# Optimization experiments

Measured on AMD Instinct MI355X. Metric: run time of the kernel, lower is better.

## Reference

```python
import jax, jax.numpy as jnp
import numpy as np

N = 200_000      # total nodes
E = 3_200_000    # directed edges
F = 128          # input features
G = 2_000        # graphs in batch
SIZES = (128, 128, 128, 128, 128, 64)
K = 2            # TAGConv hops
EPS = 1e-5


def setup_inputs() -> dict:
    key = jax.random.key(0)
    ks = jax.random.split(key, 12)
    x = jax.random.normal(ks[0], (N, F), jnp.float32)
    edge_index = jax.random.randint(ks[1], (2, E), 0, N, dtype=jnp.int32).astype(jnp.int64)
    segment_ids = jnp.sort(jax.random.randint(ks[2], (N,), 0, G, dtype=jnp.int32)).astype(jnp.int64)
    conv_W = jax.random.normal(ks[3], (5, (K + 1) * 128, 128), jnp.float32) * 0.05
    conv_W_last = jax.random.normal(ks[4], ((K + 1) * 128, 64), jnp.float32) * 0.05
    bn_gamma = jnp.ones((5, 128), jnp.float32)
    bn_beta = jnp.zeros((5, 128), jnp.float32)
    bn_gamma_last = jnp.ones((64,), jnp.float32)
    bn_beta_last = jnp.zeros((64,), jnp.float32)
    agg_bn_gamma = jnp.ones((4,), jnp.float32)
    agg_bn_beta = jnp.zeros((4,), jnp.float32)
    agg_W = jax.random.normal(ks[5], (64, 4 * 64), jnp.float32) * 0.05
    agg_b = jnp.zeros((64,), jnp.float32)
    out_W = jax.random.normal(ks[6], (1, 64), jnp.float32) * 0.05
    out_b = jnp.zeros((1,), jnp.float32)
    return dict(x=x, edge_index=edge_index, segment_ids=segment_ids, conv_W=conv_W,
                conv_W_last=conv_W_last, bn_gamma=bn_gamma, bn_beta=bn_beta,
                bn_gamma_last=bn_gamma_last, bn_beta_last=bn_beta_last,
                agg_bn_gamma=agg_bn_gamma, agg_bn_beta=agg_bn_beta,
                agg_W=agg_W, agg_b=agg_b, out_W=out_W, out_b=out_b)


def _forward(x, edge_index, segment_ids, conv_W, conv_W_last, bn_gamma, bn_beta,
             bn_gamma_last, bn_beta_last, agg_bn_gamma, agg_bn_beta,
             agg_W, agg_b, out_W, out_b):
    src, dst = edge_index[0], edge_index[1]
    deg = jax.ops.segment_sum(jnp.ones((E,), x.dtype), dst, num_segments=N)
    norm = jnp.where(deg > 0, jax.lax.rsqrt(jnp.maximum(deg, 1.0)), 0.0)[:, None]  # D^{-1/2}

    def prop(h):  # h: [N, d] -> D^{-1/2} A D^{-1/2} h
        return norm * jax.ops.segment_sum((h * norm)[src], dst, num_segments=N)

    def tagconv(h, W):  # concat of A_norm^k h for k=0..K, then linear (no bias; BN follows)
        hs = [h]
        for _ in range(K):
            hs.append(prop(hs[-1]))
        return jnp.concatenate(hs, axis=-1) @ W

    def bn(h, g, b):  # training-mode batchnorm over nodes
        m = h.mean(0)
        v = h.var(0)
        return (h - m) * jax.lax.rsqrt(v + EPS) * g + b

    outs = []
    h = x
    for l in range(len(SIZES)):
        if l < 5:
            W, g, b = conv_W[l], bn_gamma[l], bn_beta[l]
        else:
            W, g, b = conv_W_last, bn_gamma_last, bn_beta_last
        h = jax.nn.relu(bn(tagconv(h, W), g, b))
        if l >= 2 and SIZES[l] == SIZES[l - 2]:  # skip connection
            h = h + outs[l - 2]
        outs.append(h)

    # ragged pooling: (max, min, mean, std) per graph
    counts = jax.ops.segment_sum(jnp.ones((N,), h.dtype), segment_ids, num_segments=G)[:, None]
    s = jax.ops.segment_sum(h, segment_ids, num_segments=G)
    mean = s / jnp.maximum(counts, 1.0)
    ssq = jax.ops.segment_sum(h * h, segment_ids, num_segments=G)
    var = (ssq - counts * mean * mean) / jnp.maximum(counts - 1.0, 1.0)  # unbiased like th.std
    std = jnp.sqrt(jnp.maximum(var, 0.0))
    mx = jax.ops.segment_max(h, segment_ids, num_segments=G)
    mn = jax.ops.segment_min(h, segment_ids, num_segments=G)
    pooled = jnp.stack([mx, mn, mean, std], axis=1)  # [G, 4, 64]

    # aggregation BatchNorm1d over the 4 pooling channels (stats over graphs x feat)
    m = pooled.mean(axis=(0, 2))
    v = pooled.var(axis=(0, 2))
    pooled = (pooled - m[None, :, None]) * jax.lax.rsqrt(v + EPS)[None, :, None] \
             * agg_bn_gamma[None, :, None] + agg_bn_beta[None, :, None]

    flat = pooled.reshape(G, 4 * SIZES[-1])
    hg = flat @ agg_W.T + agg_b           # aggregation Linear(256 -> 64)
    return hg @ out_W.T + out_b           # output Linear(64 -> 1), shape [G, 1]


def reference(x, edge_index, segment_ids, conv_W, conv_W_last, bn_gamma, bn_beta,
              bn_gamma_last, bn_beta_last, agg_bn_gamma, agg_bn_beta,
              agg_W, agg_b, out_W, out_b):
    return _forward(x, edge_index, segment_ids, conv_W, conv_W_last, bn_gamma, bn_beta,
                    bn_gamma_last, bn_beta_last, agg_bn_gamma, agg_bn_beta,
                    agg_W, agg_b, out_W, out_b)
```

## Files before the change

### kernel.cpp

```cpp
#include <hip/hip_runtime.h>
#include <cstddef>
#include <cstdint>

#define N_NODES  200000
#define N_EDGES  3200000
#define N_GRAPHS 2000
#define BN_EPS   1e-5f
#define NB       391
#define BSH      9
#define CHUNK    16384

typedef unsigned int   u32;
typedef unsigned short u16;

using short8   = __attribute__((ext_vector_type(8))) short;
using floatx16 = __attribute__((ext_vector_type(16))) float;

__device__ __forceinline__ float bflo(u32 v) { union {u32 i; float f;} c; c.i = v << 16; return c.f; }
__device__ __forceinline__ float bfhi(u32 v) { union {u32 i; float f;} c; c.i = v & 0xffff0000u; return c.f; }
__device__ __forceinline__ float bf1(u16 v)  { union {u32 i; float f;} c; c.i = ((u32)v) << 16; return c.f; }
__device__ __forceinline__ u32 f2bf(float f) {
    union {float f; u32 i;} c; c.f = f;
    return (c.i + 0x7fffu + ((c.i >> 16) & 1u)) >> 16;
}
__device__ __forceinline__ u32 pack2(float a, float b) { return f2bf(a) | (f2bf(b) << 16); }

__global__ void x2bf_kernel(const float* __restrict__ x, u16* __restrict__ xb, int total4) {
    for (int i = blockIdx.x * 256 + threadIdx.x; i < total4; i += gridDim.x * 256) {
        float4 v = ((const float4*)x)[i];
        uint2 o; o.x = pack2(v.x, v.y); o.y = pack2(v.z, v.w);
        ((uint2*)xb)[i] = o;
    }
}

__global__ void wpack_all(const float* __restrict__ convW, const float* __restrict__ convWlast,
                          u16* __restrict__ whi, u16* __restrict__ wlo) {
    const int PER = 384 * 128;
    int tid = blockIdx.x * 256 + threadIdx.x;
    float w;
    int dst;
    if (tid < 5 * PER) {
        int l = tid / PER, r = tid % PER;
        int k = r / 128, nn = r % 128;
        w = convW[tid];
        dst = l * PER + (k >> 6) * 128 * 64 + nn * 64 + (k & 63);
    } else {
        int r = tid - 5 * PER;
        if (r >= 384 * 64) return;
        int k = r / 64, nn = r % 64;
        w = convWlast[r];
        dst = 5 * PER + (k >> 6) * 64 * 64 + nn * 64 + (k & 63);
    }
    u16 hi = (u16)f2bf(w);
    float rem = w - bf1(hi);
    whi[dst] = hi;
    wlo[dst] = (u16)f2bf(rem);
}

__global__ __launch_bounds__(256)
void bucket_hist(const int* __restrict__ edst, int* __restrict__ bcnt, int e) {
    __shared__ int h[NB];
    for (int t = threadIdx.x; t < NB; t += 256) h[t] = 0;
    __syncthreads();
    int base = blockIdx.x * CHUNK;
    int end  = min(base + CHUNK, e);
    for (int i = base + threadIdx.x; i < end; i += 256)
        atomicAdd(&h[edst[i] >> BSH], 1);
    __syncthreads();
    for (int t = threadIdx.x; t < NB; t += 256)
        if (h[t]) atomicAdd(&bcnt[t], h[t]);
}

__global__ void bucket_scan(const int* __restrict__ bcnt, int* __restrict__ bbase,
                            int* __restrict__ bcur) {
    __shared__ int ls[512];
    int t = threadIdx.x;
    int v = (t < NB) ? bcnt[t] : 0;
    ls[t] = v;
    __syncthreads();
    for (int off = 1; off < 512; off <<= 1) {
        int a = (t >= off) ? ls[t - off] : 0;
        __syncthreads();
        ls[t] += a;
        __syncthreads();
    }
    if (t <= NB) {
        int excl = ls[t] - v;
        bbase[t] = excl;
        if (t < NB) bcur[t] = excl;
    }
}

__global__ __launch_bounds__(256)
void bucket_scatter(const int* __restrict__ esrc, const int* __restrict__ edst,
                    int* __restrict__ bcur, uint2* __restrict__ esorted, int e) {
    __shared__ int h[NB], lbase[NB], lcur[NB];
    for (int t = threadIdx.x; t < NB; t += 256) { h[t] = 0; lcur[t] = 0; }
    __syncthreads();
    int base = blockIdx.x * CHUNK;
    int end  = min(base + CHUNK, e);
    for (int i = base + threadIdx.x; i < end; i += 256)
        atomicAdd(&h[edst[i] >> BSH], 1);
    __syncthreads();
    for (int t = threadIdx.x; t < NB; t += 256)
        lbase[t] = h[t] ? atomicAdd(&bcur[t], h[t]) : 0;
    __syncthreads();
    for (int i = base + threadIdx.x; i < end; i += 256) {
        int d = edst[i];
        int b = d >> BSH;
        int p = lbase[b] + atomicAdd(&lcur[b], 1);
        uint2 ed; ed.x = (u32)esrc[i]; ed.y = (u32)d;
        esorted[p] = ed;
    }
}

__global__ __launch_bounds__(256)
void bucket_fill(const uint2* __restrict__ esorted, const int* __restrict__ bbase,
                 int* __restrict__ rowptr, int* __restrict__ csr,
                 float* __restrict__ normv, int n, int e) {
    __shared__ int cnt[512], loc[512], tsum[256];
    const int b = blockIdx.x;
    const int ebeg = bbase[b], eend = bbase[b + 1];
    const int t = threadIdx.x;
    cnt[t] = 0; cnt[t + 256] = 0;
    __syncthreads();
    for (int i = ebeg + t; i < eend; i += 256)
        atomicAdd(&cnt[esorted[i].y & 511], 1);
    __syncthreads();
    int c0 = cnt[2 * t], c1 = cnt[2 * t + 1];
    tsum[t] = c0 + c1;
    __syncthreads();
    for (int off = 1; off < 256; off <<= 1) {
        int a = (t >= off) ? tsum[t - off] : 0;
        __syncthreads();
        tsum[t] += a;
        __syncthreads();
    }
    int excl = tsum[t] - (c0 + c1);
    loc[2 * t] = excl;
    loc[2 * t + 1] = excl + c0;
    __syncthreads();
    for (int j = t; j < 512; j += 256) {
        int node = (b << 9) + j;
        if (node < n) {
            rowptr[node] = ebeg + loc[j];
            int deg = cnt[j];
            normv[node] = (deg > 0) ? rsqrtf((float)deg) : 0.f;
        }
    }
    if (b == 0 && t == 0) rowptr[n] = e;
    __syncthreads();
    for (int j = t; j < 512; j += 256) cnt[j] = loc[j];
    __syncthreads();
    for (int i = ebeg + t; i < eend; i += 256) {
        uint2 ed = esorted[i];
        int slot = ebeg + atomicAdd(&cnt[ed.y & 511], 1);
        csr[slot] = (int)ed.x;
    }
}

__global__ __launch_bounds__(256)
void prop_kernel(const u16* __restrict__ hin, const float* __restrict__ norm,
                 const int* __restrict__ rowptr, const int* __restrict__ csr,
                 u16* __restrict__ pout, int n) {
    int wave = threadIdx.x >> 6;
    int lane = threadIdx.x & 63;
    int node = blockIdx.x * 4 + wave;
    if (node >= n) return;
    const int q = lane >> 4;
    const int f = (lane & 15) * 8;
    int s = rowptr[node], e = rowptr[node + 1];
    float a0 = 0, a1 = 0, a2 = 0, a3 = 0, a4 = 0, a5 = 0, a6 = 0, a7 = 0;
    int i = s + q;
    if (i + 12 < e) {
        int sn0 = csr[i], sn1 = csr[i + 4], sn2 = csr[i + 8], sn3 = csr[i + 12];
        while (true) {
            float nw0 = norm[sn0], nw1 = norm[sn1], nw2 = norm[sn2], nw3 = norm[sn3];
            uint4 v0 = *(const uint4*)(hin + (size_t)sn0 * 128 + f);
            uint4 v1 = *(const uint4*)(hin + (size_t)sn1 * 128 + f);
            uint4 v2 = *(const uint4*)(hin + (size_t)sn2 * 128 + f);
            uint4 v3 = *(const uint4*)(hin + (size_t)sn3 * 128 + f);
            int ni = i + 16;
            bool more = (ni + 12 < e);
            int t0 = 0, t1 = 0, t2 = 0, t3 = 0;
            if (more) {
                t0 = csr[ni]; t1 = csr[ni + 4]; t2 = csr[ni + 8]; t3 = csr[ni + 12];
            }
            a0 += bflo(v0.x) * nw0 + bflo(v1.x) * nw1 + bflo(v2.x) * nw2 + bflo(v3.x) * nw3;
            a1 += bfhi(v0.x) * nw0 + bfhi(v1.x) * nw1 + bfhi(v2.x) * nw2 + bfhi(v3.x) * nw3;
            a2 += bflo(v0.y) * nw0 + bflo(v1.y) * nw1 + bflo(v2.y) * nw2 + bflo(v3.y) * nw3;
            a3 += bfhi(v0.y) * nw0 + bfhi(v1.y) * nw1 + bfhi(v2.y) * nw2 + bfhi(v3.y) * nw3;
            a4 += bflo(v0.z) * nw0 + bflo(v1.z) * nw1 + bflo(v2.z) * nw2 + bflo(v3.z) * nw3;
            a5 += bfhi(v0.z) * nw0 + bfhi(v1.z) * nw1 + bfhi(v2.z) * nw2 + bfhi(v3.z) * nw3;
            a6 += bflo(v0.w) * nw0 + bflo(v1.w) * nw1 + bflo(v2.w) * nw2 + bflo(v3.w) * nw3;
            a7 += bfhi(v0.w) * nw0 + bfhi(v1.w) * nw1 + bfhi(v2.w) * nw2 + bfhi(v3.w) * nw3;
            i = ni;
            if (!more) break;
            sn0 = t0; sn1 = t1; sn2 = t2; sn3 = t3;
        }
    }
    for (; i < e; i += 4) {
        int sn0 = csr[i];
        float nw0 = norm[sn0];
        uint4 v0 = *(const uint4*)(hin + (size_t)sn0 * 128 + f);
        a0 += bflo(v0.x) * nw0; a1 += bfhi(v0.x) * nw0;
        a2 += bflo(v0.y) * nw0; a3 += bfhi(v0.y) * nw0;
        a4 += bflo(v0.z) * nw0; a5 += bfhi(v0.z) * nw0;
        a6 += bflo(v0.w) * nw0; a7 += bfhi(v0.w) * nw0;
    }
    a0 += __shfl_down(a0, 32, 64); a1 += __shfl_down(a1, 32, 64);
    a2 += __shfl_down(a2, 32, 64); a3 += __shfl_down(a3, 32, 64);
    a4 += __shfl_down(a4, 32, 64); a5 += __shfl_down(a5, 32, 64);
    a6 += __shfl_down(a6, 32, 64); a7 += __shfl_down(a7, 32, 64);
    a0 += __shfl_down(a0, 16, 64); a1 += __shfl_down(a1, 16, 64);
    a2 += __shfl_down(a2, 16, 64); a3 += __shfl_down(a3, 16, 64);
    a4 += __shfl_down(a4, 16, 64); a5 += __shfl_down(a5, 16, 64);
    a6 += __shfl_down(a6, 16, 64); a7 += __shfl_down(a7, 16, 64);
    if (q == 0) {
        float nd = norm[node];
        uint4 o;
        o.x = pack2(a0 * nd, a1 * nd);
        o.y = pack2(a2 * nd, a3 * nd);
        o.z = pack2(a4 * nd, a5 * nd);
        o.w = pack2(a6 * nd, a7 * nd);
        *(uint4*)(pout + (size_t)node * 128 + f) = o;
    }
}

template <int DOUT>
__global__ __launch_bounds__(256)
void gemm_mfma(const u16* __restrict__ A0, const u16* __restrict__ A1,
               const u16* __restrict__ A2, const u16* __restrict__ whi,
               const u16* __restrict__ wlo, u16* __restrict__ outp,
               float* __restrict__ gstats, int n) {
    constexpr int TJ = DOUT / 64;
    constexpr int BELEMS = DOUT * 64;
    __shared__ u16 As[128 * 64];
    __shared__ u16 Bh[BELEMS];
    __shared__ u16 Bl[BELEMS];
    __shared__ float col_s[DOUT];
    __shared__ float col_q[DOUT];

    const int tid  = threadIdx.x;
    const int wave = tid >> 6;
    const int lane = tid & 63;
    const int wrow = wave >> 1;
    const int wcol = wave & 1;
    const int row0 = blockIdx.x * 128;
    const int m    = lane & 31;
    const int half = lane >> 5;

    const u16* mats[3] = {A0, A1, A2};

    floatx16 acc[2][TJ];
#pragma unroll
    for (int ti = 0; ti < 2; ++ti)
#pragma unroll
        for (int tj = 0; tj < TJ; ++tj)
#pragma unroll
            for (int r = 0; r < 16; ++r) acc[ti][tj][r] = 0.f;

    for (int c = 0; c < 6; ++c) {
        const u16* M = mats[c >> 1];
        const int kloc = (c & 1) * 64;
#pragma unroll
        for (int it = 0; it < 4; ++it) {
            int rib  = wave * 32 + it * 8 + (lane >> 3);
            int grow = row0 + rib;
            if (grow >= n) grow = n - 1;
            uint4 v = *(const uint4*)(M + (size_t)grow * 128 + kloc + (lane & 7) * 8);
            int cc = (lane & 7) ^ (rib & 7);
            *(uint4*)&As[rib * 64 + cc * 8] = v;
        }
        {
            const int cbase = c * BELEMS;
#pragma unroll
            for (int j = 0; j < BELEMS / 2048; ++j) {
                int idx  = tid + j * 256;
                int nrow = idx >> 3, seg = idx & 7;
                int dcc  = seg ^ (nrow & 7);
                *(uint4*)&Bh[nrow * 64 + dcc * 8] =
                    *(const uint4*)(whi + cbase + idx * 8);
                *(uint4*)&Bl[nrow * 64 + dcc * 8] =
                    *(const uint4*)(wlo + cbase + idx * 8);
            }
        }
        __syncthreads();
#pragma unroll
        for (int s = 0; s < 4; ++s) {
            const int cc = s * 2 + half;
            short8 a[2], bhf[TJ], blf[TJ];
#pragma unroll
            for (int ti = 0; ti < 2; ++ti) {
                int r = wrow * 64 + ti * 32 + m;
                a[ti] = *(const short8*)&As[r * 64 + ((cc ^ (r & 7)) * 8)];
            }
#pragma unroll
            for (int tj = 0; tj < TJ; ++tj) {
                int rr = wcol * TJ * 32 + tj * 32 + m;
                int off = rr * 64 + ((cc ^ (rr & 7)) * 8);
                bhf[tj] = *(const short8*)&Bh[off];
                blf[tj] = *(const short8*)&Bl[off];
            }
#pragma unroll
            for (int ti = 0; ti < 2; ++ti)
#pragma unroll
                for (int tj = 0; tj < TJ; ++tj) {
                    acc[ti][tj] = __builtin_amdgcn_mfma_f32_32x32x16_bf16(
                        a[ti], bhf[tj], acc[ti][tj], 0, 0, 0);
                    acc[ti][tj] = __builtin_amdgcn_mfma_f32_32x32x16_bf16(
                        a[ti], blf[tj], acc[ti][tj], 0, 0, 0);
                }
        }
        __syncthreads();
    }

    if (tid < DOUT) { col_s[tid] = 0.f; col_q[tid] = 0.f; }
    __syncthreads();
#pragma unroll
    for (int tj = 0; tj < TJ; ++tj) {
        int gcol = (wcol * TJ + tj) * 32 + m;
        float s = 0.f, qq = 0.f;
#pragma unroll
        for (int ti = 0; ti < 2; ++ti)
#pragma unroll
            for (int r = 0; r < 16; ++r) {
                int grow = row0 + wrow * 64 + ti * 32 + (r & 3) + 8 * (r >> 2) + 4 * half;
                if (grow < n) {
                    float v = acc[ti][tj][r];
                    s += v; qq += v * v;
                    outp[(size_t)grow * DOUT + gcol] = (u16)f2bf(v);
                }
            }
        atomicAdd(&col_s[gcol], s);
        atomicAdd(&col_q[gcol], qq);
    }
    __syncthreads();
    if (tid < DOUT) {
        atomicAdd(&gstats[tid], col_s[tid]);
        atomicAdd(&gstats[DOUT + tid], col_q[tid]);
    }
}

template <int DOUT, bool SKIP>
__global__ __launch_bounds__(256)
void bn_apply(u16* __restrict__ h, const float* __restrict__ stats,
              const float* __restrict__ gamma, const float* __restrict__ beta,
              const u16* __restrict__ skip, int total4, float inv_n) {
    constexpr int C4 = DOUT / 4;
    __shared__ float sh_scale[DOUT], sh_shift[DOUT];
    if (threadIdx.x < DOUT) {
        int t = threadIdx.x;
        float mm = stats[t] * inv_n;
        float var = stats[DOUT + t] * inv_n - mm * mm;
        float sc = rsqrtf(var + BN_EPS) * gamma[t];
        sh_scale[t] = sc;
        sh_shift[t] = beta[t] - mm * sc;
    }
    __syncthreads();
    for (int idx = blockIdx.x * 256 + threadIdx.x; idx < total4; idx += gridDim.x * 256) {
        int c4 = (idx % C4) * 4;
        uint2 u = ((const uint2*)h)[idx];
        float v0 = bflo(u.x), v1 = bfhi(u.x), v2 = bflo(u.y), v3 = bfhi(u.y);
        v0 = fmaxf(fmaf(v0, sh_scale[c4 + 0], sh_shift[c4 + 0]), 0.f);
        v1 = fmaxf(fmaf(v1, sh_scale[c4 + 1], sh_shift[c4 + 1]), 0.f);
        v2 = fmaxf(fmaf(v2, sh_scale[c4 + 2], sh_shift[c4 + 2]), 0.f);
        v3 = fmaxf(fmaf(v3, sh_scale[c4 + 3], sh_shift[c4 + 3]), 0.f);
        if (SKIP) {
            uint2 sk = ((const uint2*)skip)[idx];
            v0 += bflo(sk.x); v1 += bfhi(sk.x); v2 += bflo(sk.y); v3 += bfhi(sk.y);
        }
        uint2 o; o.x = pack2(v0, v1); o.y = pack2(v2, v3);
        ((uint2*)h)[idx] = o;
    }
}

__global__ void gstart_kernel(const int* __restrict__ seg, int* __restrict__ gstart,
                              int n, int g_count) {
    int i = blockIdx.x * 256 + threadIdx.x;
    if (i >= n) return;
    int cur = seg[i];
    if (i == 0) {
        for (int g = 0; g <= cur; ++g) gstart[g] = 0;
    } else {
        int prev = seg[i - 1];
        for (int g = prev + 1; g <= cur; ++g) gstart[g] = i;
    }
    if (i == n - 1) {
        for (int g = cur + 1; g <= g_count; ++g) gstart[g] = n;
    }
}

__global__ __launch_bounds__(256)
void pool_kernel(const u16* __restrict__ hraw, const float* __restrict__ stats,
                 const float* __restrict__ gamma, const float* __restrict__ beta,
                 const int* __restrict__ gstart, float* __restrict__ pooled,
                 int g_count, float inv_n) {
    int wave = threadIdx.x >> 6;
    int lane = threadIdx.x & 63;
    int g = blockIdx.x * 4 + wave;
    if (g >= g_count) return;
    float mmean = stats[lane] * inv_n;
    float var = stats[64 + lane] * inv_n - mmean * mmean;
    float sc = rsqrtf(var + BN_EPS) * gamma[lane];
    float sh = beta[lane] - mmean * sc;
    int s = gstart[g], e = gstart[g + 1];
    float mx = -INFINITY, mn = INFINITY, sm = 0.f, sq = 0.f;
    for (int nidx = s; nidx < e; ++nidx) {
        float v = fmaxf(fmaf(bf1(hraw[(size_t)nidx * 64 + lane]), sc, sh), 0.f);
        mx = fmaxf(mx, v);
        mn = fminf(mn, v);
        sm += v;
        sq += v * v;
    }
    float cnt = (float)(e - s);
    float mean = sm / fmaxf(cnt, 1.f);
    float var2 = (sq - cnt * mean * mean) / fmaxf(cnt - 1.f, 1.f);
    float sd = sqrtf(fmaxf(var2, 0.f));
    size_t base = (size_t)g * 256;
    pooled[base + 0 * 64 + lane] = mx;
    pooled[base + 1 * 64 + lane] = mn;
    pooled[base + 2 * 64 + lane] = mean;
    pooled[base + 3 * 64 + lane] = sd;
}

__global__ void agg_stats(const float* __restrict__ pooled, float* __restrict__ aggstat,
                          int g_count) {
    int ch = blockIdx.x;
    int total = g_count * 64;
    float s = 0.f, q = 0.f;
    for (int i = threadIdx.x; i < total; i += 256) {
        int g = i >> 6, f = i & 63;
        float v = pooled[(size_t)g * 256 + ch * 64 + f];
        s += v; q += v * v;
    }
    __shared__ float ls[256], lq[256];
    ls[threadIdx.x] = s; lq[threadIdx.x] = q;
    __syncthreads();
    for (int off = 128; off > 0; off >>= 1) {
        if (threadIdx.x < off) {
            ls[threadIdx.x] += ls[threadIdx.x + off];
            lq[threadIdx.x] += lq[threadIdx.x + off];
        }
        __syncthreads();
    }
    if (threadIdx.x == 0) {
        float inv = 1.f / (float)total;
        float m = ls[0] * inv;
        aggstat[ch * 2 + 0] = m;
        aggstat[ch * 2 + 1] = lq[0] * inv - m * m;
    }
}

__global__ __launch_bounds__(256)
void final_kernel(const float* __restrict__ pooled, const float* __restrict__ aggstat,
                  const float* __restrict__ agg_gamma, const float* __restrict__ agg_beta,
                  const float* __restrict__ aggW, const float* __restrict__ aggb,
                  const float* __restrict__ outW, const float* __restrict__ outb,
                  float* __restrict__ out, int g_count) {
    __shared__ float sflat[4][256];
    int wave = threadIdx.x >> 6;
    int lane = threadIdx.x & 63;
    int g = blockIdx.x * 4 + wave;
    if (g < g_count) {
#pragma unroll
        for (int c = 0; c < 4; ++c) {
            float v = pooled[(size_t)g * 256 + c * 64 + lane];
            float m = aggstat[c * 2], var = aggstat[c * 2 + 1];
            v = (v - m) * rsqrtf(var + BN_EPS) * agg_gamma[c] + agg_beta[c];
            sflat[wave][c * 64 + lane] = v;
        }
    }
    __syncthreads();
    if (g < g_count) {
        float acc = aggb[lane];
        const float* wrow = aggW + lane * 256;
#pragma unroll 8
        for (int i = 0; i < 256; ++i)
            acc = fmaf(sflat[wave][i], wrow[i], acc);
        float t = acc * outW[lane];
        for (int off = 32; off > 0; off >>= 1) t += __shfl_down(t, off, 64);
        if (lane == 0) out[g] = t + outb[0];
    }
}

extern "C" void kernel_launch(void* const* d_in, const int* in_sizes, int n_in,
                              void* d_out, int out_size, void* d_ws, size_t ws_size,
                              hipStream_t stream) {
    const int N = N_NODES, E = N_EDGES, G = N_GRAPHS;

    const float* x           = (const float*)d_in[0];
    const int*   ei          = (const int*)d_in[1];
    const int*   seg         = (const int*)d_in[2];
    const float* conv_W      = (const float*)d_in[3];
    const float* conv_W_last = (const float*)d_in[4];
    const float* bn_g        = (const float*)d_in[5];
    const float* bn_b        = (const float*)d_in[6];
    const float* bn_gl       = (const float*)d_in[7];
    const float* bn_bl       = (const float*)d_in[8];
    const float* agg_g       = (const float*)d_in[9];
    const float* agg_bt      = (const float*)d_in[10];
    const float* aggW        = (const float*)d_in[11];
    const float* aggb        = (const float*)d_in[12];
    const float* outW        = (const float*)d_in[13];
    const float* outb        = (const float*)d_in[14];
    float* out = (float*)d_out;

    const int* esrc = ei;
    const int* edst = ei + E;

    size_t off = 0;
    auto alloc = [&](size_t bytes) -> void* {
        void* p = (char*)d_ws + off;
        off += (bytes + 255) & ~(size_t)255;
        return p;
    };
    float* normv  = (float*)alloc((size_t)N * 4);
    int*   rowptr = (int*)alloc((size_t)(N + 1) * 4);
    int*   csr    = (int*)alloc((size_t)E * 4);
    int*   bcnt   = (int*)alloc((NB + 1) * 4);
    int*   bbase  = (int*)alloc((NB + 1) * 4);
    int*   bcur   = (int*)alloc((NB + 1) * 4);
    int*   gstart = (int*)alloc((size_t)(G + 1) * 4);
    float* statsA = (float*)alloc(6 * 256 * 4);
    float* aggstat= (float*)alloc(8 * 4);
    float* pooled = (float*)alloc((size_t)G * 256 * 4);
    const size_t WPACK = 5 * 384 * 128 + 384 * 64;
    u16*   whip   = (u16*)alloc(WPACK * 2);
    u16*   wlop   = (u16*)alloc(WPACK * 2);
    u16*   ring0  = (u16*)alloc((size_t)N * 128 * 2);
    u16*   ring1  = (u16*)alloc((size_t)N * 128 * 2);
    u16*   ring2  = (u16*)alloc((size_t)N * 128 * 2);
    u16*   p1     = (u16*)alloc((size_t)N * 128 * 2);
    u16*   p2     = (u16*)alloc((size_t)N * 128 * 2);
    u16*   ring[3] = {ring0, ring1, ring2};
    uint2* esorted = (uint2*)p2;

    hipMemsetAsync(bcnt, 0, (NB + 1) * 4, stream);
    hipMemsetAsync(statsA, 0, 6 * 256 * 4, stream);
    const int nchunk = (E + CHUNK - 1) / CHUNK;
    bucket_hist<<<nchunk, 256, 0, stream>>>(edst, bcnt, E);
    bucket_scan<<<1, 512, 0, stream>>>(bcnt, bbase, bcur);
    bucket_scatter<<<nchunk, 256, 0, stream>>>(esrc, edst, bcur, esorted, E);
    bucket_fill<<<NB, 256, 0, stream>>>(esorted, bbase, rowptr, csr, normv, N, E);

    x2bf_kernel<<<2048, 256, 0, stream>>>(x, ring2, N * 128 / 4);

    wpack_all<<<(5 * 384 * 128 + 384 * 64 + 255) / 256, 256, 0, stream>>>(
        conv_W, conv_W_last, whip, wlop);

    gstart_kernel<<<(N + 255) / 256, 256, 0, stream>>>(seg, gstart, N, G);

    const u16* h_in = ring2;
    const int gemm_grid = (N + 127) / 128;
    const float inv_n = 1.f / (float)N;
    for (int l = 0; l < 6; ++l) {
        const int dout = (l < 5) ? 128 : 64;
        const u16* whi = whip + (size_t)((l < 5) ? l * 384 * 128 : 5 * 384 * 128);
        const u16* wlo = wlop + (size_t)((l < 5) ? l * 384 * 128 : 5 * 384 * 128);
        const float* gamma = (l < 5) ? (bn_g + l * 128) : bn_gl;
        const float* beta  = (l < 5) ? (bn_b + l * 128) : bn_bl;
        float* stats = statsA + l * 256;
        u16* outbuf = ring[l % 3];

        prop_kernel<<<(N + 3) / 4, 256, 0, stream>>>(h_in, normv, rowptr, csr, p1, N);
        prop_kernel<<<(N + 3) / 4, 256, 0, stream>>>(p1, normv, rowptr, csr, p2, N);

        if (dout == 128)
            gemm_mfma<128><<<gemm_grid, 256, 0, stream>>>(h_in, p1, p2, whi, wlo, outbuf,
                                                          stats, N);
        else
            gemm_mfma<64><<<gemm_grid, 256, 0, stream>>>(h_in, p1, p2, whi, wlo, outbuf,
                                                         stats, N);

        if (l < 5) {
            int total4 = N * dout / 4;
            bool has_skip = (l >= 2);
            const u16* skipb = has_skip ? ring[(l - 2) % 3] : nullptr;
            if (has_skip)
                bn_apply<128, true><<<8192, 256, 0, stream>>>(outbuf, stats, gamma, beta,
                                                              skipb, total4, inv_n);
            else
                bn_apply<128, false><<<8192, 256, 0, stream>>>(outbuf, stats, gamma, beta,
                                                               nullptr, total4, inv_n);
        }
        h_in = outbuf;
    }

    pool_kernel<<<(G + 3) / 4, 256, 0, stream>>>(ring[5 % 3], statsA + 5 * 256,
                                                 bn_gl, bn_bl, gstart, pooled, G, inv_n);
    agg_stats<<<4, 256, 0, stream>>>(pooled, aggstat, G);
    final_kernel<<<(G + 3) / 4, 256, 0, stream>>>(pooled, aggstat, agg_g, agg_bt,
                                                  aggW, aggb, outW, outb, out, G);
}
```

Measured before the change: 2.728 ms.

## Split SpMM propagation into two feature-half passes for better cache locality

Each propagation is split into two kernel launches, each covering 64 of the 128 bf16 features. Within a wave, 8 lanes cover one 128-byte half-row and 8 edges are processed in parallel. The aim is to halve the gathered working set per pass so more of the source feature matrix stays in L2/MALL during the random gathers. In exchange, the CSR indices and norms are read twice, kernel launches double, and each wave covers fewer bytes per edge.

After: 3.114 ms. 1.14x slower.

```diff
diff --git a/kernel.cpp b/kernel.cpp
--- a/kernel.cpp
+++ b/kernel.cpp
@@ -160,53 +160,58 @@
 }
 
 __global__ __launch_bounds__(256)
-void prop_kernel(const u16* __restrict__ hin, const float* __restrict__ norm,
-                 const int* __restrict__ rowptr, const int* __restrict__ csr,
-                 u16* __restrict__ pout, int n) {
+void prop_half(const u16* __restrict__ hin, const float* __restrict__ norm,
+               const int* __restrict__ rowptr, const int* __restrict__ csr,
+               u16* __restrict__ pout, int n, int foff) {
     int wave = threadIdx.x >> 6;
     int lane = threadIdx.x & 63;
     int node = blockIdx.x * 4 + wave;
     if (node >= n) return;
-    const int q = lane >> 4;
-    const int f = (lane & 15) * 8;
+    const int e8 = lane >> 3;
+    const int f  = foff + (lane & 7) * 8;
     int s = rowptr[node], e = rowptr[node + 1];
     float a0 = 0, a1 = 0, a2 = 0, a3 = 0, a4 = 0, a5 = 0, a6 = 0, a7 = 0;
-    int i = s + q;
-    if (i + 12 < e) {
-        int sn0 = csr[i], sn1 = csr[i + 4], sn2 = csr[i + 8], sn3 = csr[i + 12];
+    int ib = s;
+    if (ib + 16 <= e) {
+        int sn0 = csr[ib + e8], sn1 = csr[ib + 8 + e8];
         while (true) {
-            float nw0 = norm[sn0], nw1 = norm[sn1], nw2 = norm[sn2], nw3 = norm[sn3];
+            float nw0 = norm[sn0], nw1 = norm[sn1];
             uint4 v0 = *(const uint4*)(hin + (size_t)sn0 * 128 + f);
             uint4 v1 = *(const uint4*)(hin + (size_t)sn1 * 128 + f);
-            uint4 v2 = *(const uint4*)(hin + (size_t)sn2 * 128 + f);
-            uint4 v3 = *(const uint4*)(hin + (size_t)sn3 * 128 + f);
-            int ni = i + 16;
-            bool more = (ni + 12 < e);
-            int t0 = 0, t1 = 0, t2 = 0, t3 = 0;
-            if (more) {
-                t0 = csr[ni]; t1 = csr[ni + 4]; t2 = csr[ni + 8]; t3 = csr[ni + 12];
-            }
-            a0 += bflo(v0.x) * nw0 + bflo(v1.x) * nw1 + bflo(v2.x) * nw2 + bflo(v3.x) * nw3;
-            a1 += bfhi(v0.x) * nw0 + bfhi(v1.x) * nw1 + bfhi(v2.x) * nw2 + bfhi(v3.x) * nw3;
-            a2 += bflo(v0.y) * nw0 + bflo(v1.y) * nw1 + bflo(v2.y) * nw2 + bflo(v3.y) * nw3;
-            a3 += bfhi(v0.y) * nw0 + bfhi(v1.y) * nw1 + bfhi(v2.y) * nw2 + bfhi(v3.y) * nw3;
-            a4 += bflo(v0.z) * nw0 + bflo(v1.z) * nw1 + bflo(v2.z) * nw2 + bflo(v3.z) * nw3;
-            a5 += bfhi(v0.z) * nw0 + bfhi(v1.z) * nw1 + bfhi(v2.z) * nw2 + bfhi(v3.z) * nw3;
-            a6 += bflo(v0.w) * nw0 + bflo(v1.w) * nw1 + bflo(v2.w) * nw2 + bflo(v3.w) * nw3;
-            a7 += bfhi(v0.w) * nw0 + bfhi(v1.w) * nw1 + bfhi(v2.w) * nw2 + bfhi(v3.w) * nw3;
-            i = ni;
+            int nb = ib + 16;
+            bool more = (nb + 16 <= e);
+            int t0 = 0, t1 = 0;
+            if (more) { t0 = csr[nb + e8]; t1 = csr[nb + 8 + e8]; }
+            a0 += bflo(v0.x) * nw0 + bflo(v1.x) * nw1;
+            a1 += bfhi(v0.x) * nw0 + bfhi(v1.x) * nw1;
+            a2 += bflo(v0.y) * nw0 + bflo(v1.y) * nw1;
+            a3 += bfhi(v0.y) * nw0 + bfhi(v1.y) * nw1;
+            a4 += bflo(v0.z) * nw0 + bflo(v1.z) * nw1;
+            a5 += bfhi(v0.z) * nw0 + bfhi(v1.z) * nw1;
+            a6 += bflo(v0.w) * nw0 + bflo(v1.w) * nw1;
+            a7 += bfhi(v0.w) * nw0 + bfhi(v1.w) * nw1;
+            ib = nb;
             if (!more) break;
-            sn0 = t0; sn1 = t1; sn2 = t2; sn3 = t3;
-        }
-    }
-    for (; i < e; i += 4) {
-        int sn0 = csr[i];
-        float nw0 = norm[sn0];
-        uint4 v0 = *(const uint4*)(hin + (size_t)sn0 * 128 + f);
-        a0 += bflo(v0.x) * nw0; a1 += bfhi(v0.x) * nw0;
-        a2 += bflo(v0.y) * nw0; a3 += bfhi(v0.y) * nw0;
-        a4 += bflo(v0.z) * nw0; a5 += bfhi(v0.z) * nw0;
-        a6 += bflo(v0.w) * nw0; a7 += bfhi(v0.w) * nw0;
+            sn0 = t0; sn1 = t1;
+        }
+    }
+    if (ib + e8 < e) {
+        int sn = csr[ib + e8];
+        float nw = norm[sn];
+        uint4 v = *(const uint4*)(hin + (size_t)sn * 128 + f);
+        a0 += bflo(v.x) * nw; a1 += bfhi(v.x) * nw;
+        a2 += bflo(v.y) * nw; a3 += bfhi(v.y) * nw;
+        a4 += bflo(v.z) * nw; a5 += bfhi(v.z) * nw;
+        a6 += bflo(v.w) * nw; a7 += bfhi(v.w) * nw;
+    }
+    if (ib + 8 + e8 < e) {
+        int sn = csr[ib + 8 + e8];
+        float nw = norm[sn];
+        uint4 v = *(const uint4*)(hin + (size_t)sn * 128 + f);
+        a0 += bflo(v.x) * nw; a1 += bfhi(v.x) * nw;
+        a2 += bflo(v.y) * nw; a3 += bfhi(v.y) * nw;
+        a4 += bflo(v.z) * nw; a5 += bfhi(v.z) * nw;
+        a6 += bflo(v.w) * nw; a7 += bfhi(v.w) * nw;
     }
     a0 += __shfl_down(a0, 32, 64); a1 += __shfl_down(a1, 32, 64);
     a2 += __shfl_down(a2, 32, 64); a3 += __shfl_down(a3, 32, 64);
@@ -216,7 +221,11 @@
     a2 += __shfl_down(a2, 16, 64); a3 += __shfl_down(a3, 16, 64);
     a4 += __shfl_down(a4, 16, 64); a5 += __shfl_down(a5, 16, 64);
     a6 += __shfl_down(a6, 16, 64); a7 += __shfl_down(a7, 16, 64);
-    if (q == 0) {
+    a0 += __shfl_down(a0, 8, 64);  a1 += __shfl_down(a1, 8, 64);
+    a2 += __shfl_down(a2, 8, 64);  a3 += __shfl_down(a3, 8, 64);
+    a4 += __shfl_down(a4, 8, 64);  a5 += __shfl_down(a5, 8, 64);
+    a6 += __shfl_down(a6, 8, 64);  a7 += __shfl_down(a7, 8, 64);
+    if (e8 == 0) {
         float nd = norm[node];
         uint4 o;
         o.x = pack2(a0 * nd, a1 * nd);
@@ -553,6 +562,7 @@
 
     const u16* h_in = ring2;
     const int gemm_grid = (N + 127) / 128;
+    const int prop_grid = (N + 3) / 4;
     const float inv_n = 1.f / (float)N;
     for (int l = 0; l < 6; ++l) {
         const int dout = (l < 5) ? 128 : 64;
@@ -563,8 +573,10 @@
         float* stats = statsA + l * 256;
         u16* outbuf = ring[l % 3];
 
-        prop_kernel<<<(N + 3) / 4, 256, 0, stream>>>(h_in, normv, rowptr, csr, p1, N);
-        prop_kernel<<<(N + 3) / 4, 256, 0, stream>>>(p1, normv, rowptr, csr, p2, N);
+        prop_half<<<prop_grid, 256, 0, stream>>>(h_in, normv, rowptr, csr, p1, N, 0);
+        prop_half<<<prop_grid, 256, 0, stream>>>(h_in, normv, rowptr, csr, p1, N, 64);
+        prop_half<<<prop_grid, 256, 0, stream>>>(p1, normv, rowptr, csr, p2, N, 0);
+        prop_half<<<prop_grid, 256, 0, stream>>>(p1, normv, rowptr, csr, p2, N, 64);
 
         if (dout == 128)
             gemm_mfma<128><<<gemm_grid, 256, 0, stream>>>(h_in, p1, p2, whi, wlo, outbuf,
```
